# Optimization experiments

Measured on AMD Instinct MI355X. Metric: run time of the kernel, lower is better.

The kernel has to match this reference:

```python
import jax, jax.numpy as jnp
import numpy as np

N = 200000
M = 100000
K = 27
C = 128
NEG_SLOPE = 0.2


def setup_inputs() -> dict:
    key = jax.random.key(0)
    ks = jax.random.split(key, 7)
    feats = jax.random.normal(ks[0], (N, C), dtype=jnp.float32)
    # small init scale (mirrors xavier * 0.1) to keep activations stable through 27-tap convs
    W1 = jax.random.normal(ks[1], (K, C, C), dtype=jnp.float32) * 0.02
    W2 = jax.random.normal(ks[2], (C, C), dtype=jnp.float32) * 0.05
    W3 = jax.random.normal(ks[3], (K, C, C), dtype=jnp.float32) * 0.02
    in_map = jax.random.randint(ks[4], (K, M), 0, N, dtype=jnp.int32)
    out_map = jax.random.randint(ks[5], (K, M), 0, N, dtype=jnp.int32)
    mask = jax.random.uniform(ks[6], (N, 1), dtype=jnp.float32)
    return {"feats": feats, "W1": W1, "W2": W2, "W3": W3,
            "in_map": in_map, "out_map": out_map, "mask": mask}


def _lrelu(x):
    return jnp.where(x >= 0, x, NEG_SLOPE * x)


def _sparse_conv(feats, W, in_map, out_map, n_out):
    """Gather-GEMM-scatter sparse conv: scan over K kernel offsets.

    feats: [N, Cin]; W: [K, Cin, Cout]; in_map/out_map: [K, M].
    """
    def body(acc, xs):
        im, om, w = xs
        y = feats[im] @ w                    # [M, Cin] @ [Cin, Cout]
        return acc.at[om].add(y), None
    out0 = jnp.zeros((n_out, W.shape[-1]), feats.dtype)
    out, _ = jax.lax.scan(body, out0, (in_map, out_map, W))
    return out


def reference(feats, W1, W2, W3, in_map, out_map, mask):
    n = feats.shape[0]
    c1 = _lrelu(_sparse_conv(feats, W1, in_map, out_map, n))   # conv1 (k=3) + LeakyReLU
    c2 = _lrelu(c1 @ W2)                                       # conv2 (k=1) + LeakyReLU
    c3 = _sparse_conv(c2, W3, in_map, out_map, n)              # conv3 (k=3)
    return c3 * mask
```

## Files before the change

### kernel.cpp

```cpp
#include <hip/hip_runtime.h>
#include <hip/hip_bf16.h>


typedef __attribute__((ext_vector_type(8))) short short8;
typedef __attribute__((ext_vector_type(4))) float f32x4;

#define CDIM 128
#define BM   128
#define NEG_SLOPE 0.2f

__device__ __forceinline__ unsigned short f2bf(float x) {
    union { float f; unsigned u; } un; un.f = x;
    unsigned r = un.u + 0x7fffu + ((un.u >> 16) & 1u);
    return (unsigned short)(r >> 16);
}

__device__ __forceinline__ float lrelu(float x) {
    return x >= 0.f ? x : NEG_SLOPE * x;
}

__device__ __forceinline__ int swz(int r, int c) {
    return (r << 7) + ((((c >> 3) ^ (r & 15)) << 3));
}

__global__ void cvt_feats_kernel(const float* __restrict__ in,
                                 unsigned short* __restrict__ out, int n4) {
    int i = blockIdx.x * blockDim.x + threadIdx.x;
    if (i >= n4) return;
    float4 v = reinterpret_cast<const float4*>(in)[i];
    ushort4 o;
    o.x = f2bf(v.x); o.y = f2bf(v.y); o.z = f2bf(v.z); o.w = f2bf(v.w);
    reinterpret_cast<ushort4*>(out)[i] = o;
}

__global__ void cvt_weights_kernel(const float* __restrict__ W1,
                                   const float* __restrict__ W2,
                                   const float* __restrict__ W3,
                                   unsigned short* __restrict__ W1t,
                                   unsigned short* __restrict__ W2t,
                                   unsigned short* __restrict__ W3t) {
    const int KW = 27 * 128 * 128;
    int t = blockIdx.x * blockDim.x + threadIdx.x;
    if (t < KW) {
        int k = t >> 14, r = t & 16383, n = r >> 7, kk = r & 127;
        W1t[t] = f2bf(W1[(k << 14) + (kk << 7) + n]);
    } else if (t < 2 * KW) {
        int t2 = t - KW;
        int k = t2 >> 14, r = t2 & 16383, n = r >> 7, kk = r & 127;
        W3t[t2] = f2bf(W3[(k << 14) + (kk << 7) + n]);
    } else if (t < 2 * KW + 16384) {
        int t2 = t - 2 * KW;
        int n = t2 >> 7, kk = t2 & 127;
        W2t[t2] = f2bf(W2[(kk << 7) + n]);
    }
}

__global__ __launch_bounds__(256, 2)
void sconv_kernel(const unsigned short* __restrict__ A,
                  const unsigned short* __restrict__ Wt,
                  const int* __restrict__ in_map,
                  const int* __restrict__ out_map,
                  float* __restrict__ out,
                  int M) {
    const int k     = blockIdx.y;
    const int mbase = blockIdx.x * BM;
    const int tid   = threadIdx.x;

    __shared__ unsigned short lA[BM * CDIM];
    __shared__ unsigned short lW[CDIM * CDIM];

    const unsigned short* wk = Wt + (size_t)k * 16384;
    #pragma unroll
    for (int i = 0; i < 8; ++i) {
        int flat = (i * 256 + tid) * 8;
        int row = flat >> 7, col = flat & 127;
        short8 v = *reinterpret_cast<const short8*>(wk + flat);
        *reinterpret_cast<short8*>(&lW[swz(row, col)]) = v;
    }

    const int* imk = in_map + (size_t)k * M;
    #pragma unroll
    for (int p = 0; p < 8; ++p) {
        int r = p * 16 + (tid >> 4);
        int c = (tid & 15) * 8;
        int m = mbase + r;
        short8 v = {0, 0, 0, 0, 0, 0, 0, 0};
        if (m < M) {
            int arow = __ldg(imk + m);
            v = *reinterpret_cast<const short8*>(A + (size_t)arow * CDIM + c);
        }
        *reinterpret_cast<short8*>(&lA[swz(r, c)]) = v;
    }
    __syncthreads();

    const int wid  = tid >> 6, lane = tid & 63;
    const int wr   = (wid >> 1) * 64, wc = (wid & 1) * 64;
    const int lrow = lane & 15, quad = lane >> 4;

    f32x4 acc[4][4];
    #pragma unroll
    for (int i = 0; i < 4; ++i)
        #pragma unroll
        for (int j = 0; j < 4; ++j)
            acc[i][j] = {0.f, 0.f, 0.f, 0.f};

    #pragma unroll
    for (int s = 0; s < 4; ++s) {
        const int kf = s * 32 + quad * 8;
        short8 a[4], b[4];
        #pragma unroll
        for (int i = 0; i < 4; ++i)
            a[i] = *reinterpret_cast<const short8*>(&lA[swz(wr + i * 16 + lrow, kf)]);
        #pragma unroll
        for (int j = 0; j < 4; ++j)
            b[j] = *reinterpret_cast<const short8*>(&lW[swz(wc + j * 16 + lrow, kf)]);
        #pragma unroll
        for (int i = 0; i < 4; ++i)
            #pragma unroll
            for (int j = 0; j < 4; ++j)
                acc[i][j] = __builtin_amdgcn_mfma_f32_16x16x32_bf16(a[i], b[j], acc[i][j], 0, 0, 0);
    }

    const int* omk = out_map + (size_t)k * M;
    #pragma unroll
    for (int i = 0; i < 4; ++i) {
        #pragma unroll
        for (int reg = 0; reg < 4; ++reg) {
            int m = mbase + wr + i * 16 + quad * 4 + reg;
            if (m < M) {
                int orow = __ldg(omk + m);
                float* dst = out + (size_t)orow * CDIM + wc + lrow;
                #pragma unroll
                for (int j = 0; j < 4; ++j)
                    unsafeAtomicAdd(dst + j * 16, acc[i][j][reg]);
            }
        }
    }
}

__global__ __launch_bounds__(256, 2)
void conv2_kernel(const float* __restrict__ c1,
                  const unsigned short* __restrict__ W2t,
                  unsigned short* __restrict__ c2,
                  int M) {
    const int mbase = blockIdx.x * BM;
    const int tid   = threadIdx.x;

    __shared__ unsigned short lA[BM * CDIM];
    __shared__ unsigned short lW[CDIM * CDIM];

    #pragma unroll
    for (int i = 0; i < 8; ++i) {
        int flat = (i * 256 + tid) * 8;
        int row = flat >> 7, col = flat & 127;
        short8 v = *reinterpret_cast<const short8*>(W2t + flat);
        *reinterpret_cast<short8*>(&lW[swz(row, col)]) = v;
    }

    #pragma unroll
    for (int p = 0; p < 8; ++p) {
        int r = p * 16 + (tid >> 4);
        int c = (tid & 15) * 8;
        int m = mbase + r;
        unsigned short vv[8];
        if (m < M) {
            const float4* src = reinterpret_cast<const float4*>(c1 + (size_t)m * CDIM + c);
            float4 x0 = src[0], x1 = src[1];
            vv[0] = f2bf(lrelu(x0.x)); vv[1] = f2bf(lrelu(x0.y));
            vv[2] = f2bf(lrelu(x0.z)); vv[3] = f2bf(lrelu(x0.w));
            vv[4] = f2bf(lrelu(x1.x)); vv[5] = f2bf(lrelu(x1.y));
            vv[6] = f2bf(lrelu(x1.z)); vv[7] = f2bf(lrelu(x1.w));
        } else {
            #pragma unroll
            for (int q = 0; q < 8; ++q) vv[q] = 0;
        }
        short8 v;
        #pragma unroll
        for (int q = 0; q < 8; ++q) v[q] = (short)vv[q];
        *reinterpret_cast<short8*>(&lA[swz(r, c)]) = v;
    }
    __syncthreads();

    const int wid  = tid >> 6, lane = tid & 63;
    const int wr   = (wid >> 1) * 64, wc = (wid & 1) * 64;
    const int lrow = lane & 15, quad = lane >> 4;

    f32x4 acc[4][4];
    #pragma unroll
    for (int i = 0; i < 4; ++i)
        #pragma unroll
        for (int j = 0; j < 4; ++j)
            acc[i][j] = {0.f, 0.f, 0.f, 0.f};

    #pragma unroll
    for (int s = 0; s < 4; ++s) {
        const int kf = s * 32 + quad * 8;
        short8 a[4], b[4];
        #pragma unroll
        for (int i = 0; i < 4; ++i)
            a[i] = *reinterpret_cast<const short8*>(&lA[swz(wr + i * 16 + lrow, kf)]);
        #pragma unroll
        for (int j = 0; j < 4; ++j)
            b[j] = *reinterpret_cast<const short8*>(&lW[swz(wc + j * 16 + lrow, kf)]);
        #pragma unroll
        for (int i = 0; i < 4; ++i)
            #pragma unroll
            for (int j = 0; j < 4; ++j)
                acc[i][j] = __builtin_amdgcn_mfma_f32_16x16x32_bf16(a[i], b[j], acc[i][j], 0, 0, 0);
    }

    #pragma unroll
    for (int i = 0; i < 4; ++i) {
        #pragma unroll
        for (int reg = 0; reg < 4; ++reg) {
            int m = mbase + wr + i * 16 + quad * 4 + reg;
            if (m < M) {
                unsigned short* dst = c2 + (size_t)m * CDIM + wc + lrow;
                #pragma unroll
                for (int j = 0; j < 4; ++j)
                    dst[j * 16] = f2bf(lrelu(acc[i][j][reg]));
            }
        }
    }
}

__global__ void mask_mul_kernel(float* __restrict__ out,
                                const float* __restrict__ mask, int n4) {
    int i = blockIdx.x * blockDim.x + threadIdx.x;
    if (i >= n4) return;
    int row = i >> 5;
    float m = mask[row];
    float4 v = reinterpret_cast<float4*>(out)[i];
    v.x *= m; v.y *= m; v.z *= m; v.w *= m;
    reinterpret_cast<float4*>(out)[i] = v;
}

extern "C" void kernel_launch(void* const* d_in, const int* in_sizes, int n_in,
                              void* d_out, int out_size, void* d_ws, size_t ws_size,
                              hipStream_t stream) {
    const float* feats   = (const float*)d_in[0];
    const float* W1      = (const float*)d_in[1];
    const float* W2      = (const float*)d_in[2];
    const float* W3      = (const float*)d_in[3];
    const int*   in_map  = (const int*)d_in[4];
    const int*   out_map = (const int*)d_in[5];
    const float* mask    = (const float*)d_in[6];
    float*       out     = (float*)d_out;

    const int K = 27;
    const int N = in_sizes[0] / CDIM;
    const int M = in_sizes[4] / K;

    unsigned short* feats_bf = (unsigned short*)d_ws;
    unsigned short* c2_bf    = feats_bf + (size_t)N * CDIM;
    unsigned short* W1t      = c2_bf + (size_t)N * CDIM;
    unsigned short* W3t      = W1t + (size_t)K * CDIM * CDIM;
    unsigned short* W2t      = W3t + (size_t)K * CDIM * CDIM;
    size_t need = ((size_t)2 * N * CDIM + (size_t)2 * K * CDIM * CDIM + CDIM * CDIM) * 2;
    if (ws_size < need) return;

    const int n4 = N * CDIM / 4;
    cvt_feats_kernel<<<(n4 + 255) / 256, 256, 0, stream>>>(feats, feats_bf, n4);
    const int wtot = 2 * K * CDIM * CDIM + CDIM * CDIM;
    cvt_weights_kernel<<<(wtot + 255) / 256, 256, 0, stream>>>(W1, W2, W3, W1t, W2t, W3t);

    hipMemsetAsync(d_out, 0, (size_t)N * CDIM * sizeof(float), stream);

    dim3 gs((M + BM - 1) / BM, K);
    sconv_kernel<<<gs, 256, 0, stream>>>(feats_bf, W1t, in_map, out_map, out, M);

    conv2_kernel<<<(N + BM - 1) / BM, 256, 0, stream>>>(out, W2t, c2_bf, N);

    hipMemsetAsync(d_out, 0, (size_t)N * CDIM * sizeof(float), stream);
    sconv_kernel<<<gs, 256, 0, stream>>>(c2_bf, W3t, in_map, out_map, out, M);

    mask_mul_kernel<<<(n4 + 255) / 256, 256, 0, stream>>>(out, mask, n4);
}
```

Baseline: 2.534 ms.

## Bin gather records by output tile and accumulate sparse conv in LDS

Adds histogram, scan and scatter passes that bucket every (in, out) pair by 64-row output tile and kernel tap. A new output-stationary kernel then gathers inputs, runs the MFMA GEMM per tap and accumulates into a shared-memory tile with LDS atomics, instead of issuing float atomics to global memory. conv2 with its LeakyReLU, and the final mask multiply, are fused into the tile epilogue, which removes the output memsets and separate passes. The cost is re-staging the weights per tap for every tile, small uneven GEMMs per bin, extra preprocessing kernels, and heavy LDS use that limits occupancy.

```diff
diff --git a/kernel.cpp b/kernel.cpp
--- a/kernel.cpp
+++ b/kernel.cpp
@@ -6,7 +6,8 @@
 typedef __attribute__((ext_vector_type(4))) float f32x4;
 
 #define CDIM 128
-#define BM   128
+#define TROWS 64
+#define KTAPS 27
 #define NEG_SLOPE 0.2f
 
 __device__ __forceinline__ unsigned short f2bf(float x) {
@@ -39,7 +40,7 @@
                                    unsigned short* __restrict__ W1t,
                                    unsigned short* __restrict__ W2t,
                                    unsigned short* __restrict__ W3t) {
-    const int KW = 27 * 128 * 128;
+    const int KW = KTAPS * CDIM * CDIM;
     int t = blockIdx.x * blockDim.x + threadIdx.x;
     if (t < KW) {
         int k = t >> 14, r = t & 16383, n = r >> 7, kk = r & 127;
@@ -48,191 +49,201 @@
         int t2 = t - KW;
         int k = t2 >> 14, r = t2 & 16383, n = r >> 7, kk = r & 127;
         W3t[t2] = f2bf(W3[(k << 14) + (kk << 7) + n]);
-    } else if (t < 2 * KW + 16384) {
+    } else if (t < 2 * KW + CDIM * CDIM) {
         int t2 = t - 2 * KW;
         int n = t2 >> 7, kk = t2 & 127;
         W2t[t2] = f2bf(W2[(kk << 7) + n]);
     }
 }
 
+__global__ void hist_kernel(const int* __restrict__ om, int* __restrict__ bins, int M) {
+    int m = blockIdx.x * 256 + threadIdx.x;
+    int k = blockIdx.y;
+    if (m >= M) return;
+    int o = om[(size_t)k * M + m];
+    atomicAdd(&bins[(o >> 6) * KTAPS + k], 1);
+}
+
+__global__ void scan_kernel(const int* __restrict__ bins, int* __restrict__ starts, int B) {
+    __shared__ int lds[1024];
+    int t = threadIdx.x;
+    int seg = (B + 1023) >> 10;
+    int base = t * seg;
+    int s = 0;
+    for (int i = 0; i < seg; ++i) { int idx = base + i; if (idx < B) s += bins[idx]; }
+    lds[t] = s;
+    __syncthreads();
+    for (int off = 1; off < 1024; off <<= 1) {
+        int v = lds[t];
+        int add = (t >= off) ? lds[t - off] : 0;
+        __syncthreads();
+        lds[t] = v + add;
+        __syncthreads();
+    }
+    int run = (t == 0) ? 0 : lds[t - 1];
+    for (int i = 0; i < seg; ++i) {
+        int idx = base + i;
+        if (idx < B) { starts[idx] = run; run += bins[idx]; }
+    }
+    if (t == 1023) starts[B] = lds[1023];
+}
+
+__global__ void scatter_kernel(const int* __restrict__ im, const int* __restrict__ om,
+                               const int* __restrict__ starts, int* __restrict__ cursor,
+                               unsigned* __restrict__ rec, int M) {
+    int m = blockIdx.x * 256 + threadIdx.x;
+    int k = blockIdx.y;
+    if (m >= M) return;
+    size_t e = (size_t)k * M + m;
+    int o = om[e];
+    int bin = (o >> 6) * KTAPS + k;
+    int pos = starts[bin] + atomicAdd(&cursor[bin], 1);
+    rec[pos] = ((unsigned)im[e] << 6) | (unsigned)(o & 63);
+}
+
 __global__ __launch_bounds__(256, 2)
-void sconv_kernel(const unsigned short* __restrict__ A,
-                  const unsigned short* __restrict__ Wt,
-                  const int* __restrict__ in_map,
-                  const int* __restrict__ out_map,
-                  float* __restrict__ out,
-                  int M) {
-    const int k     = blockIdx.y;
-    const int mbase = blockIdx.x * BM;
-    const int tid   = threadIdx.x;
-
-    __shared__ unsigned short lA[BM * CDIM];
+void sconv_inv_kernel(const unsigned short* __restrict__ A,
+                      const unsigned short* __restrict__ Wt,
+                      const unsigned* __restrict__ rec,
+                      const int* __restrict__ starts,
+                      const unsigned short* __restrict__ W2t,
+                      unsigned short* __restrict__ c2,
+                      const float* __restrict__ mask,
+                      float* __restrict__ outp,
+                      int mode) {
+    __shared__ float          accW[TROWS * CDIM];
+    __shared__ unsigned short lA[TROWS * CDIM];
     __shared__ unsigned short lW[CDIM * CDIM];
 
-    const unsigned short* wk = Wt + (size_t)k * 16384;
+    const int t    = blockIdx.x;
+    const int tid  = threadIdx.x;
+    const int w    = tid >> 6;
+    const int lane = tid & 63;
+    const int lrow = lane & 15;
+    const int quad = lane >> 4;
+
     #pragma unroll
-    for (int i = 0; i < 8; ++i) {
-        int flat = (i * 256 + tid) * 8;
-        int row = flat >> 7, col = flat & 127;
-        short8 v = *reinterpret_cast<const short8*>(wk + flat);
-        *reinterpret_cast<short8*>(&lW[swz(row, col)]) = v;
-    }
-
-    const int* imk = in_map + (size_t)k * M;
-    #pragma unroll
-    for (int p = 0; p < 8; ++p) {
-        int r = p * 16 + (tid >> 4);
-        int c = (tid & 15) * 8;
-        int m = mbase + r;
-        short8 v = {0, 0, 0, 0, 0, 0, 0, 0};
-        if (m < M) {
-            int arow = __ldg(imk + m);
-            v = *reinterpret_cast<const short8*>(A + (size_t)arow * CDIM + c);
-        }
-        *reinterpret_cast<short8*>(&lA[swz(r, c)]) = v;
+    for (int i = 0; i < 8; ++i)
+        reinterpret_cast<float4*>(accW)[i * 256 + tid] = make_float4(0.f, 0.f, 0.f, 0.f);
+
+    for (int k = 0; k < KTAPS; ++k) {
+        __syncthreads();
+        const unsigned short* wk = Wt + (size_t)k * (CDIM * CDIM);
+        #pragma unroll
+        for (int i = 0; i < 8; ++i) {
+            int flat = (i * 256 + tid) * 8;
+            int row = flat >> 7, col = flat & 127;
+            *reinterpret_cast<short8*>(&lW[swz(row, col)]) =
+                *reinterpret_cast<const short8*>(wk + flat);
+        }
+        const int bin = t * KTAPS + k;
+        const int s0  = starts[bin];
+        const int cnt = starts[bin + 1] - s0;
+
+        for (int base = 0; base < cnt; base += TROWS) {
+            int c = cnt - base; if (c > TROWS) c = TROWS;
+            if (base > 0) __syncthreads();
+            #pragma unroll
+            for (int p = 0; p < 4; ++p) {
+                int r = p * 16 + (tid >> 4);
+                if (r < c) {
+                    unsigned rv = rec[s0 + base + r];
+                    int src = (int)(rv >> 6);
+                    *reinterpret_cast<short8*>(&lA[swz(r, (tid & 15) * 8)]) =
+                        *reinterpret_cast<const short8*>(A + (size_t)src * CDIM + (tid & 15) * 8);
+                }
+            }
+            __syncthreads();
+            int r16 = (c + 15) >> 4;
+            short8 b0[4], b1[4];
+            #pragma unroll
+            for (int kf = 0; kf < 4; ++kf) {
+                b0[kf] = *reinterpret_cast<const short8*>(&lW[swz(w * 32 + lrow,      kf * 32 + quad * 8)]);
+                b1[kf] = *reinterpret_cast<const short8*>(&lW[swz(w * 32 + 16 + lrow, kf * 32 + quad * 8)]);
+            }
+            for (int rt = 0; rt < r16; ++rt) {
+                f32x4 acc0 = {0.f, 0.f, 0.f, 0.f}, acc1 = {0.f, 0.f, 0.f, 0.f};
+                #pragma unroll
+                for (int kf = 0; kf < 4; ++kf) {
+                    short8 av = *reinterpret_cast<const short8*>(&lA[swz(rt * 16 + lrow, kf * 32 + quad * 8)]);
+                    acc0 = __builtin_amdgcn_mfma_f32_16x16x32_bf16(av, b0[kf], acc0, 0, 0, 0);
+                    acc1 = __builtin_amdgcn_mfma_f32_16x16x32_bf16(av, b1[kf], acc1, 0, 0, 0);
+                }
+                #pragma unroll
+                for (int reg = 0; reg < 4; ++reg) {
+                    int rr = rt * 16 + quad * 4 + reg;
+                    if (rr < c) {
+                        int slot = (int)(rec[s0 + base + rr] & 63u);
+                        atomicAdd(&accW[slot * CDIM + w * 32 + lrow],      acc0[reg]);
+                        atomicAdd(&accW[slot * CDIM + w * 32 + 16 + lrow], acc1[reg]);
+                    }
+                }
+            }
+        }
     }
     __syncthreads();
 
-    const int wid  = tid >> 6, lane = tid & 63;
-    const int wr   = (wid >> 1) * 64, wc = (wid & 1) * 64;
-    const int lrow = lane & 15, quad = lane >> 4;
-
-    f32x4 acc[4][4];
-    #pragma unroll
-    for (int i = 0; i < 4; ++i)
-        #pragma unroll
-        for (int j = 0; j < 4; ++j)
-            acc[i][j] = {0.f, 0.f, 0.f, 0.f};
-
-    #pragma unroll
-    for (int s = 0; s < 4; ++s) {
-        const int kf = s * 32 + quad * 8;
-        short8 a[4], b[4];
-        #pragma unroll
-        for (int i = 0; i < 4; ++i)
-            a[i] = *reinterpret_cast<const short8*>(&lA[swz(wr + i * 16 + lrow, kf)]);
-        #pragma unroll
-        for (int j = 0; j < 4; ++j)
-            b[j] = *reinterpret_cast<const short8*>(&lW[swz(wc + j * 16 + lrow, kf)]);
-        #pragma unroll
-        for (int i = 0; i < 4; ++i)
-            #pragma unroll
-            for (int j = 0; j < 4; ++j)
-                acc[i][j] = __builtin_amdgcn_mfma_f32_16x16x32_bf16(a[i], b[j], acc[i][j], 0, 0, 0);
-    }
-
-    const int* omk = out_map + (size_t)k * M;
-    #pragma unroll
-    for (int i = 0; i < 4; ++i) {
-        #pragma unroll
-        for (int reg = 0; reg < 4; ++reg) {
-            int m = mbase + wr + i * 16 + quad * 4 + reg;
-            if (m < M) {
-                int orow = __ldg(omk + m);
-                float* dst = out + (size_t)orow * CDIM + wc + lrow;
-                #pragma unroll
-                for (int j = 0; j < 4; ++j)
-                    unsafeAtomicAdd(dst + j * 16, acc[i][j][reg]);
-            }
-        }
-    }
-}
-
-__global__ __launch_bounds__(256, 2)
-void conv2_kernel(const float* __restrict__ c1,
-                  const unsigned short* __restrict__ W2t,
-                  unsigned short* __restrict__ c2,
-                  int M) {
-    const int mbase = blockIdx.x * BM;
-    const int tid   = threadIdx.x;
-
-    __shared__ unsigned short lA[BM * CDIM];
-    __shared__ unsigned short lW[CDIM * CDIM];
-
-    #pragma unroll
-    for (int i = 0; i < 8; ++i) {
-        int flat = (i * 256 + tid) * 8;
-        int row = flat >> 7, col = flat & 127;
-        short8 v = *reinterpret_cast<const short8*>(W2t + flat);
-        *reinterpret_cast<short8*>(&lW[swz(row, col)]) = v;
-    }
-
-    #pragma unroll
-    for (int p = 0; p < 8; ++p) {
-        int r = p * 16 + (tid >> 4);
-        int c = (tid & 15) * 8;
-        int m = mbase + r;
-        unsigned short vv[8];
-        if (m < M) {
-            const float4* src = reinterpret_cast<const float4*>(c1 + (size_t)m * CDIM + c);
-            float4 x0 = src[0], x1 = src[1];
-            vv[0] = f2bf(lrelu(x0.x)); vv[1] = f2bf(lrelu(x0.y));
-            vv[2] = f2bf(lrelu(x0.z)); vv[3] = f2bf(lrelu(x0.w));
-            vv[4] = f2bf(lrelu(x1.x)); vv[5] = f2bf(lrelu(x1.y));
-            vv[6] = f2bf(lrelu(x1.z)); vv[7] = f2bf(lrelu(x1.w));
-        } else {
-            #pragma unroll
-            for (int q = 0; q < 8; ++q) vv[q] = 0;
-        }
-        short8 v;
-        #pragma unroll
-        for (int q = 0; q < 8; ++q) v[q] = (short)vv[q];
-        *reinterpret_cast<short8*>(&lA[swz(r, c)]) = v;
-    }
-    __syncthreads();
-
-    const int wid  = tid >> 6, lane = tid & 63;
-    const int wr   = (wid >> 1) * 64, wc = (wid & 1) * 64;
-    const int lrow = lane & 15, quad = lane >> 4;
-
-    f32x4 acc[4][4];
-    #pragma unroll
-    for (int i = 0; i < 4; ++i)
-        #pragma unroll
-        for (int j = 0; j < 4; ++j)
-            acc[i][j] = {0.f, 0.f, 0.f, 0.f};
-
-    #pragma unroll
-    for (int s = 0; s < 4; ++s) {
-        const int kf = s * 32 + quad * 8;
-        short8 a[4], b[4];
-        #pragma unroll
-        for (int i = 0; i < 4; ++i)
-            a[i] = *reinterpret_cast<const short8*>(&lA[swz(wr + i * 16 + lrow, kf)]);
-        #pragma unroll
-        for (int j = 0; j < 4; ++j)
-            b[j] = *reinterpret_cast<const short8*>(&lW[swz(wc + j * 16 + lrow, kf)]);
-        #pragma unroll
-        for (int i = 0; i < 4; ++i)
-            #pragma unroll
-            for (int j = 0; j < 4; ++j)
-                acc[i][j] = __builtin_amdgcn_mfma_f32_16x16x32_bf16(a[i], b[j], acc[i][j], 0, 0, 0);
-    }
-
-    #pragma unroll
-    for (int i = 0; i < 4; ++i) {
-        #pragma unroll
-        for (int reg = 0; reg < 4; ++reg) {
-            int m = mbase + wr + i * 16 + quad * 4 + reg;
-            if (m < M) {
-                unsigned short* dst = c2 + (size_t)m * CDIM + wc + lrow;
-                #pragma unroll
-                for (int j = 0; j < 4; ++j)
-                    dst[j * 16] = f2bf(lrelu(acc[i][j][reg]));
-            }
-        }
-    }
-}
-
-__global__ void mask_mul_kernel(float* __restrict__ out,
-                                const float* __restrict__ mask, int n4) {
-    int i = blockIdx.x * blockDim.x + threadIdx.x;
-    if (i >= n4) return;
-    int row = i >> 5;
-    float m = mask[row];
-    float4 v = reinterpret_cast<float4*>(out)[i];
-    v.x *= m; v.y *= m; v.z *= m; v.w *= m;
-    reinterpret_cast<float4*>(out)[i] = v;
+    if (mode == 1) {
+        #pragma unroll
+        for (int i = 0; i < 8; ++i) {
+            int flat = (i * 256 + tid) * 8;
+            int row = flat >> 7, col = flat & 127;
+            *reinterpret_cast<short8*>(&lW[swz(row, col)]) =
+                *reinterpret_cast<const short8*>(W2t + flat);
+        }
+        {
+            int row = tid >> 2, c0 = (tid & 3) * 32;
+            #pragma unroll
+            for (int j = 0; j < 4; ++j) {
+                const float4* sp = reinterpret_cast<const float4*>(accW + row * CDIM + c0 + j * 8);
+                float4 x0 = sp[0], x1 = sp[1];
+                short8 v;
+                v[0] = (short)f2bf(lrelu(x0.x)); v[1] = (short)f2bf(lrelu(x0.y));
+                v[2] = (short)f2bf(lrelu(x0.z)); v[3] = (short)f2bf(lrelu(x0.w));
+                v[4] = (short)f2bf(lrelu(x1.x)); v[5] = (short)f2bf(lrelu(x1.y));
+                v[6] = (short)f2bf(lrelu(x1.z)); v[7] = (short)f2bf(lrelu(x1.w));
+                *reinterpret_cast<short8*>(&lA[swz(row, c0 + j * 8)]) = v;
+            }
+        }
+        __syncthreads();
+        unsigned short* cacc = reinterpret_cast<unsigned short*>(accW);
+        #pragma unroll
+        for (int rt = 0; rt < 4; ++rt) {
+            f32x4 acc0 = {0.f, 0.f, 0.f, 0.f}, acc1 = {0.f, 0.f, 0.f, 0.f};
+            #pragma unroll
+            for (int kf = 0; kf < 4; ++kf) {
+                short8 av = *reinterpret_cast<const short8*>(&lA[swz(rt * 16 + lrow, kf * 32 + quad * 8)]);
+                short8 b0 = *reinterpret_cast<const short8*>(&lW[swz(w * 32 + lrow,      kf * 32 + quad * 8)]);
+                short8 b1 = *reinterpret_cast<const short8*>(&lW[swz(w * 32 + 16 + lrow, kf * 32 + quad * 8)]);
+                acc0 = __builtin_amdgcn_mfma_f32_16x16x32_bf16(av, b0, acc0, 0, 0, 0);
+                acc1 = __builtin_amdgcn_mfma_f32_16x16x32_bf16(av, b1, acc1, 0, 0, 0);
+            }
+            #pragma unroll
+            for (int reg = 0; reg < 4; ++reg) {
+                int rr = rt * 16 + quad * 4 + reg;
+                cacc[rr * CDIM + w * 32 + lrow]      = f2bf(lrelu(acc0[reg]));
+                cacc[rr * CDIM + w * 32 + 16 + lrow] = f2bf(lrelu(acc1[reg]));
+            }
+        }
+        __syncthreads();
+        #pragma unroll
+        for (int i = 0; i < 4; ++i) {
+            int flat = (i * 256 + tid) * 8;
+            *reinterpret_cast<short8*>(c2 + (size_t)t * TROWS * CDIM + flat) =
+                *reinterpret_cast<const short8*>(cacc + flat);
+        }
+    } else {
+        int row = tid >> 2, c0 = (tid & 3) * 32;
+        float mval = mask[t * TROWS + row];
+        const float4* sp = reinterpret_cast<const float4*>(accW + row * CDIM + c0);
+        float4* dp = reinterpret_cast<float4*>(outp + (size_t)t * TROWS * CDIM + row * CDIM + c0);
+        #pragma unroll
+        for (int j = 0; j < 8; ++j) {
+            float4 v = sp[j];
+            v.x *= mval; v.y *= mval; v.z *= mval; v.w *= mval;
+            dp[j] = v;
+        }
+    }
 }
 
 extern "C" void kernel_launch(void* const* d_in, const int* in_sizes, int n_in,
@@ -247,32 +258,38 @@
     const float* mask    = (const float*)d_in[6];
     float*       out     = (float*)d_out;
 
-    const int K = 27;
-    const int N = in_sizes[0] / CDIM;
-    const int M = in_sizes[4] / K;
-
-    unsigned short* feats_bf = (unsigned short*)d_ws;
-    unsigned short* c2_bf    = feats_bf + (size_t)N * CDIM;
-    unsigned short* W1t      = c2_bf + (size_t)N * CDIM;
-    unsigned short* W3t      = W1t + (size_t)K * CDIM * CDIM;
-    unsigned short* W2t      = W3t + (size_t)K * CDIM * CDIM;
-    size_t need = ((size_t)2 * N * CDIM + (size_t)2 * K * CDIM * CDIM + CDIM * CDIM) * 2;
-    if (ws_size < need) return;
+    const int N  = in_sizes[0] / CDIM;
+    const int M  = in_sizes[4] / KTAPS;
+    const int NT = (N + TROWS - 1) / TROWS;
+    const int B  = NT * KTAPS;
+    const size_t E = (size_t)KTAPS * M;
+
+    char* p = (char*)d_ws;
+    auto take = [&](size_t bytes) { char* r = p; p += (bytes + 15) & ~(size_t)15; return r; };
+    unsigned short* feats_bf = (unsigned short*)take((size_t)N * CDIM * 2);
+    unsigned short* c2_bf    = (unsigned short*)take((size_t)N * CDIM * 2);
+    unsigned short* W1t      = (unsigned short*)take((size_t)KTAPS * CDIM * CDIM * 2);
+    unsigned short* W3t      = (unsigned short*)take((size_t)KTAPS * CDIM * CDIM * 2);
+    unsigned short* W2t      = (unsigned short*)take((size_t)CDIM * CDIM * 2);
+    int*            bins     = (int*)take((size_t)(B + 1) * 4);
+    int*            starts   = (int*)take((size_t)(B + 1) * 4);
+    unsigned*       rec      = (unsigned*)take(E * 4);
+    if ((size_t)(p - (char*)d_ws) > ws_size) return;
 
     const int n4 = N * CDIM / 4;
     cvt_feats_kernel<<<(n4 + 255) / 256, 256, 0, stream>>>(feats, feats_bf, n4);
-    const int wtot = 2 * K * CDIM * CDIM + CDIM * CDIM;
+    const int wtot = 2 * KTAPS * CDIM * CDIM + CDIM * CDIM;
     cvt_weights_kernel<<<(wtot + 255) / 256, 256, 0, stream>>>(W1, W2, W3, W1t, W2t, W3t);
 
-    hipMemsetAsync(d_out, 0, (size_t)N * CDIM * sizeof(float), stream);
-
-    dim3 gs((M + BM - 1) / BM, K);
-    sconv_kernel<<<gs, 256, 0, stream>>>(feats_bf, W1t, in_map, out_map, out, M);
-
-    conv2_kernel<<<(N + BM - 1) / BM, 256, 0, stream>>>(out, W2t, c2_bf, N);
-
-    hipMemsetAsync(d_out, 0, (size_t)N * CDIM * sizeof(float), stream);
-    sconv_kernel<<<gs, 256, 0, stream>>>(c2_bf, W3t, in_map, out_map, out, M);
-
-    mask_mul_kernel<<<(n4 + 255) / 256, 256, 0, stream>>>(out, mask, n4);
-}
+    hipMemsetAsync(bins, 0, (size_t)(B + 1) * 4, stream);
+    dim3 gm((M + 255) / 256, KTAPS);
+    hist_kernel<<<gm, 256, 0, stream>>>(out_map, bins, M);
+    scan_kernel<<<1, 1024, 0, stream>>>(bins, starts, B);
+    hipMemsetAsync(bins, 0, (size_t)(B + 1) * 4, stream);
+    scatter_kernel<<<gm, 256, 0, stream>>>(in_map, out_map, starts, bins, rec, M);
+
+    sconv_inv_kernel<<<NT, 256, 0, stream>>>(feats_bf, W1t, rec, starts,
+                                             W2t, c2_bf, nullptr, nullptr, 1);
+    sconv_inv_kernel<<<NT, 256, 0, stream>>>(c2_bf, W3t, rec, starts,
+                                             nullptr, nullptr, mask, out, 2);
+}
```

After: 4.864 ms. 1.92x slower.

## Replace atomic scatter with sorted-record segmented reduction over bf16 per-tap GEMM outputs

Applied to the files above, without the earlier changes.

Replaces the float atomic scatter-add with a deterministic pipeline. A histogram, scan and scatter build a CSR list of contributions per output row, grouped by tap chunks. The per-tap GEMMs write bf16 results to a workspace buffer, and a row-wise reduce kernel sums each output row's contributions, with mask multiply and a channel permutation folded into the final pass. This is meant to remove atomic contention and the extra memset and mask passes. In exchange it adds preprocessing kernels, a large intermediate write/read, and extra bf16 rounding of partial products.

```diff
diff --git a/kernel.cpp b/kernel.cpp
--- a/kernel.cpp
+++ b/kernel.cpp
@@ -6,7 +6,7 @@
 typedef __attribute__((ext_vector_type(4))) float f32x4;
 
 #define CDIM 128
-#define BM   128
+#define KTAPS 27
 #define NEG_SLOPE 0.2f
 
 __device__ __forceinline__ unsigned short f2bf(float x) {
@@ -14,14 +14,11 @@
     unsigned r = un.u + 0x7fffu + ((un.u >> 16) & 1u);
     return (unsigned short)(r >> 16);
 }
-
-__device__ __forceinline__ float lrelu(float x) {
-    return x >= 0.f ? x : NEG_SLOPE * x;
-}
-
-__device__ __forceinline__ int swz(int r, int c) {
-    return (r << 7) + ((((c >> 3) ^ (r & 15)) << 3));
-}
+__device__ __forceinline__ float bflo(unsigned v) { union { unsigned u; float f; } un; un.u = v << 16; return un.f; }
+__device__ __forceinline__ float bfhi(unsigned v) { union { unsigned u; float f; } un; un.u = v & 0xffff0000u; return un.f; }
+__device__ __forceinline__ float lrelu(float x) { return x >= 0.f ? x : NEG_SLOPE * x; }
+__device__ __forceinline__ int swz(int r, int c) { return (r << 7) + ((((c >> 3) ^ (r & 15)) << 3)); }
+__device__ __forceinline__ int pcol(int q) { return (q & 64) | ((q & 3) << 4) | ((q >> 2) & 15); }
 
 __global__ void cvt_feats_kernel(const float* __restrict__ in,
                                  unsigned short* __restrict__ out, int n4) {
@@ -38,35 +35,81 @@
                                    const float* __restrict__ W3,
                                    unsigned short* __restrict__ W1t,
                                    unsigned short* __restrict__ W2t,
-                                   unsigned short* __restrict__ W3t) {
-    const int KW = 27 * 128 * 128;
+                                   unsigned short* __restrict__ W3t, int perm) {
+    const int KW = KTAPS * CDIM * CDIM;
     int t = blockIdx.x * blockDim.x + threadIdx.x;
     if (t < KW) {
         int k = t >> 14, r = t & 16383, n = r >> 7, kk = r & 127;
         W1t[t] = f2bf(W1[(k << 14) + (kk << 7) + n]);
     } else if (t < 2 * KW) {
         int t2 = t - KW;
-        int k = t2 >> 14, r = t2 & 16383, n = r >> 7, kk = r & 127;
+        int k = t2 >> 14, r = t2 & 16383, n = r >> 7, q = r & 127;
+        int kk = perm ? pcol(q) : q;
         W3t[t2] = f2bf(W3[(k << 14) + (kk << 7) + n]);
-    } else if (t < 2 * KW + 16384) {
+    } else if (t < 2 * KW + CDIM * CDIM) {
         int t2 = t - 2 * KW;
-        int n = t2 >> 7, kk = t2 & 127;
+        int n = t2 >> 7, q = t2 & 127;
+        int kk = perm ? pcol(q) : q;
         W2t[t2] = f2bf(W2[(kk << 7) + n]);
     }
 }
 
+__global__ void hist_kernel(const int* __restrict__ om, int* __restrict__ bins,
+                            int M, int ng, int g) {
+    int m = blockIdx.x * 256 + threadIdx.x;
+    int k = blockIdx.y;
+    if (m >= M) return;
+    int o = om[(size_t)k * M + m];
+    atomicAdd(&bins[o * ng + k / g], 1);
+}
+
+__global__ void scan_kernel(const int* __restrict__ bins, int* __restrict__ starts, int B) {
+    __shared__ int lds[1024];
+    int t = threadIdx.x;
+    int seg = (B + 1023) >> 10;
+    int base = t * seg;
+    int s = 0;
+    for (int i = 0; i < seg; ++i) { int idx = base + i; if (idx < B) s += bins[idx]; }
+    lds[t] = s;
+    __syncthreads();
+    for (int off = 1; off < 1024; off <<= 1) {
+        int v = lds[t];
+        int add = (t >= off) ? lds[t - off] : 0;
+        __syncthreads();
+        lds[t] = v + add;
+        __syncthreads();
+    }
+    int run = (t == 0) ? 0 : lds[t - 1];
+    for (int i = 0; i < seg; ++i) {
+        int idx = base + i;
+        if (idx < B) { starts[idx] = run; run += bins[idx]; }
+    }
+    if (t == 1023) starts[B] = lds[1023];
+}
+
+__global__ void scatter_kernel(const int* __restrict__ om,
+                               const int* __restrict__ starts, int* __restrict__ cursor,
+                               unsigned* __restrict__ rec, int M, int ng, int g) {
+    int m = blockIdx.x * 256 + threadIdx.x;
+    int k = blockIdx.y;
+    if (m >= M) return;
+    int o = om[(size_t)k * M + m];
+    int bin = o * ng + k / g;
+    int pos = starts[bin] + atomicAdd(&cursor[bin], 1);
+    rec[pos] = (unsigned)(k * M + m);
+}
+
 __global__ __launch_bounds__(256, 2)
-void sconv_kernel(const unsigned short* __restrict__ A,
-                  const unsigned short* __restrict__ Wt,
-                  const int* __restrict__ in_map,
-                  const int* __restrict__ out_map,
-                  float* __restrict__ out,
-                  int M) {
-    const int k     = blockIdx.y;
-    const int mbase = blockIdx.x * BM;
+void gemm_gather_kernel(const unsigned short* __restrict__ A,
+                        const unsigned short* __restrict__ Wt,
+                        const int* __restrict__ in_map,
+                        unsigned short* __restrict__ Y,
+                        int M, int klo) {
+    const int k     = klo + blockIdx.y;
+    const int mbase = blockIdx.x * 128;
     const int tid   = threadIdx.x;
 
-    __shared__ unsigned short lA[BM * CDIM];
+    __shared__ unsigned short lA[128 * CDIM];
     __shared__ unsigned short lW[CDIM * CDIM];
 
     const unsigned short* wk = Wt + (size_t)k * 16384;
@@ -74,10 +117,9 @@
     for (int i = 0; i < 8; ++i) {
         int flat = (i * 256 + tid) * 8;
         int row = flat >> 7, col = flat & 127;
-        short8 v = *reinterpret_cast<const short8*>(wk + flat);
-        *reinterpret_cast<short8*>(&lW[swz(row, col)]) = v;
-    }
-
+        *reinterpret_cast<short8*>(&lW[swz(row, col)]) =
+            *reinterpret_cast<const short8*>(wk + flat);
+    }
     const int* imk = in_map + (size_t)k * M;
     #pragma unroll
     for (int p = 0; p < 8; ++p) {
@@ -93,8 +135,214 @@
     }
     __syncthreads();
 
-    const int wid  = tid >> 6, lane = tid & 63;
-    const int wr   = (wid >> 1) * 64, wc = (wid & 1) * 64;
+    const int wid = tid >> 6, lane = tid & 63;
+    const int wr = (wid >> 1) * 64, wc = (wid & 1) * 64;
+    const int lrow = lane & 15, quad = lane >> 4;
+
+    f32x4 acc[4][4];
+    #pragma unroll
+    for (int i = 0; i < 4; ++i)
+        #pragma unroll
+        for (int j = 0; j < 4; ++j)
+            acc[i][j] = {0.f, 0.f, 0.f, 0.f};
+
+    #pragma unroll
+    for (int s = 0; s < 4; ++s) {
+        const int kf = s * 32 + quad * 8;
+        short8 a[4], b[4];
+        #pragma unroll
+        for (int i = 0; i < 4; ++i)
+            a[i] = *reinterpret_cast<const short8*>(&lA[swz(wr + i * 16 + lrow, kf)]);
+        #pragma unroll
+        for (int j = 0; j < 4; ++j)
+            b[j] = *reinterpret_cast<const short8*>(&lW[swz(wc + j * 16 + lrow, kf)]);
+        #pragma unroll
+        for (int i = 0; i < 4; ++i)
+            #pragma unroll
+            for (int j = 0; j < 4; ++j)
+                acc[i][j] = __builtin_amdgcn_mfma_f32_16x16x32_bf16(a[i], b[j], acc[i][j], 0, 0, 0);
+    }
+
+    const size_t ybase = (size_t)(k - klo) * M;
+    #pragma unroll
+    for (int i = 0; i < 4; ++i) {
+        #pragma unroll
+        for (int reg = 0; reg < 4; ++reg) {
+            int m = mbase + wr + i * 16 + quad * 4 + reg;
+            if (m < M) {
+                ushort4 pk;
+                pk.x = f2bf(acc[i][0][reg]);
+                pk.y = f2bf(acc[i][1][reg]);
+                pk.z = f2bf(acc[i][2][reg]);
+                pk.w = f2bf(acc[i][3][reg]);
+                *reinterpret_cast<ushort4*>(Y + (ybase + m) * CDIM + wc + lrow * 4) = pk;
+            }
+        }
+    }
+}
+
+__global__ void reduce_kernel(const unsigned short* __restrict__ Y,
+                              const unsigned* __restrict__ rec,
+                              const int* __restrict__ starts,
+                              float* __restrict__ acc,
+                              const float* __restrict__ mask,
+                              int N, int ng, int grp, unsigned eoff,
+                              int first, int final_mask) {
+    int row = blockIdx.x * 4 + (threadIdx.x >> 6);
+    if (row >= N) return;
+    int lane = threadIdx.x & 63;
+    int bin = row * ng + grp;
+    int s0 = starts[bin], cnt = starts[bin + 1] - s0;
+    float a0 = 0.f, a1 = 0.f;
+    if (!first) {
+        float2 p = *reinterpret_cast<const float2*>(acc + (size_t)row * CDIM + 2 * lane);
+        a0 = p.x; a1 = p.y;
+    }
+    const unsigned* rp = rec + s0;
+    int c = 0;
+    for (; c + 4 <= cnt; c += 4) {
+        unsigned e0 = rp[c] - eoff, e1 = rp[c + 1] - eoff;
+        unsigned e2 = rp[c + 2] - eoff, e3 = rp[c + 3] - eoff;
+        unsigned v0 = *reinterpret_cast<const unsigned*>(Y + (size_t)e0 * CDIM + 2 * lane);
+        unsigned v1 = *reinterpret_cast<const unsigned*>(Y + (size_t)e1 * CDIM + 2 * lane);
+        unsigned v2 = *reinterpret_cast<const unsigned*>(Y + (size_t)e2 * CDIM + 2 * lane);
+        unsigned v3 = *reinterpret_cast<const unsigned*>(Y + (size_t)e3 * CDIM + 2 * lane);
+        a0 += (bflo(v0) + bflo(v1)) + (bflo(v2) + bflo(v3));
+        a1 += (bfhi(v0) + bfhi(v1)) + (bfhi(v2) + bfhi(v3));
+    }
+    for (; c < cnt; ++c) {
+        unsigned e = rp[c] - eoff;
+        unsigned v = *reinterpret_cast<const unsigned*>(Y + (size_t)e * CDIM + 2 * lane);
+        a0 += bflo(v); a1 += bfhi(v);
+    }
+    if (!final_mask) {
+        *reinterpret_cast<float2*>(acc + (size_t)row * CDIM + 2 * lane) = make_float2(a0, a1);
+    } else {
+        float mv = mask[row];
+        acc[(size_t)row * CDIM + pcol(2 * lane)]     = a0 * mv;
+        acc[(size_t)row * CDIM + pcol(2 * lane + 1)] = a1 * mv;
+    }
+}
+
+__global__ __launch_bounds__(256, 2)
+void conv2_perm_kernel(const float* __restrict__ c1,
+                       const unsigned short* __restrict__ W2t,
+                       unsigned short* __restrict__ c2,
+                       int N) {
+    const int mbase = blockIdx.x * 128;
+    const int tid   = threadIdx.x;
+
+    __shared__ unsigned short lA[128 * CDIM];
+    __shared__ unsigned short lW[CDIM * CDIM];
+
+    #pragma unroll
+    for (int i = 0; i < 8; ++i) {
+        int flat = (i * 256 + tid) * 8;
+        int row = flat >> 7, col = flat & 127;
+        *reinterpret_cast<short8*>(&lW[swz(row, col)]) =
+            *reinterpret_cast<const short8*>(W2t + flat);
+    }
+    #pragma unroll
+    for (int p = 0; p < 8; ++p) {
+        int r = p * 16 + (tid >> 4);
+        int c = (tid & 15) * 8;
+        int m = mbase + r;
+        short8 v = {0, 0, 0, 0, 0, 0, 0, 0};
+        if (m < N) {
+            const float4* src = reinterpret_cast<const float4*>(c1 + (size_t)m * CDIM + c);
+            float4 x0 = src[0], x1 = src[1];
+            v[0] = (short)f2bf(lrelu(x0.x)); v[1] = (short)f2bf(lrelu(x0.y));
+            v[2] = (short)f2bf(lrelu(x0.z)); v[3] = (short)f2bf(lrelu(x0.w));
+            v[4] = (short)f2bf(lrelu(x1.x)); v[5] = (short)f2bf(lrelu(x1.y));
+            v[6] = (short)f2bf(lrelu(x1.z)); v[7] = (short)f2bf(lrelu(x1.w));
+        }
+        *reinterpret_cast<short8*>(&lA[swz(r, c)]) = v;
+    }
+    __syncthreads();
+
+    const int wid = tid >> 6, lane = tid & 63;
+    const int wr = (wid >> 1) * 64, wc = (wid & 1) * 64;
+    const int lrow = lane & 15, quad = lane >> 4;
+
+    f32x4 acc[4][4];
+    #pragma unroll
+    for (int i = 0; i < 4; ++i)
+        #pragma unroll
+        for (int j = 0; j < 4; ++j)
+            acc[i][j] = {0.f, 0.f, 0.f, 0.f};
+
+    #pragma unroll
+    for (int s = 0; s < 4; ++s) {
+        const int kf = s * 32 + quad * 8;
+        short8 a[4], b[4];
+        #pragma unroll
+        for (int i = 0; i < 4; ++i)
+            a[i] = *reinterpret_cast<const short8*>(&lA[swz(wr + i * 16 + lrow, kf)]);
+        #pragma unroll
+        for (int j = 0; j < 4; ++j)
+            b[j] = *reinterpret_cast<const short8*>(&lW[swz(wc + j * 16 + lrow, kf)]);
+        #pragma unroll
+        for (int i = 0; i < 4; ++i)
+            #pragma unroll
+            for (int j = 0; j < 4; ++j)
+                acc[i][j] = __builtin_amdgcn_mfma_f32_16x16x32_bf16(a[i], b[j], acc[i][j], 0, 0, 0);
+    }
+
+    #pragma unroll
+    for (int i = 0; i < 4; ++i) {
+        #pragma unroll
+        for (int reg = 0; reg < 4; ++reg) {
+            int m = mbase + wr + i * 16 + quad * 4 + reg;
+            if (m < N) {
+                ushort4 pk;
+                pk.x = f2bf(lrelu(acc[i][0][reg]));
+                pk.y = f2bf(lrelu(acc[i][1][reg]));
+                pk.z = f2bf(lrelu(acc[i][2][reg]));
+                pk.w = f2bf(lrelu(acc[i][3][reg]));
+                *reinterpret_cast<ushort4*>(c2 + (size_t)m * CDIM + wc + lrow * 4) = pk;
+            }
+        }
+    }
+}
+
+__global__ __launch_bounds__(256, 2)
+void sconv_atomic_kernel(const unsigned short* __restrict__ A,
+                         const unsigned short* __restrict__ Wt,
+                         const int* __restrict__ in_map,
+                         const int* __restrict__ out_map,
+                         float* __restrict__ out, int M) {
+    const int k     = blockIdx.y;
+    const int mbase = blockIdx.x * 128;
+    const int tid   = threadIdx.x;
+
+    __shared__ unsigned short lA[128 * CDIM];
+    __shared__ unsigned short lW[CDIM * CDIM];
+
+    const unsigned short* wk = Wt + (size_t)k * 16384;
+    #pragma unroll
+    for (int i = 0; i < 8; ++i) {
+        int flat = (i * 256 + tid) * 8;
+        int row = flat >> 7, col = flat & 127;
+        *reinterpret_cast<short8*>(&lW[swz(row, col)]) =
+            *reinterpret_cast<const short8*>(wk + flat);
+    }
+    const int* imk = in_map + (size_t)k * M;
+    #pragma unroll
+    for (int p = 0; p < 8; ++p) {
+        int r = p * 16 + (tid >> 4);
+        int c = (tid & 15) * 8;
+        int m = mbase + r;
+        short8 v = {0, 0, 0, 0, 0, 0, 0, 0};
+        if (m < M) {
+            int arow = __ldg(imk + m);
+            v = *reinterpret_cast<const short8*>(A + (size_t)arow * CDIM + c);
+        }
+        *reinterpret_cast<short8*>(&lA[swz(r, c)]) = v;
+    }
+    __syncthreads();
+
+    const int wid = tid >> 6, lane = tid & 63;
+    const int wr = (wid >> 1) * 64, wc = (wid & 1) * 64;
     const int lrow = lane & 15, quad = lane >> 4;
 
     f32x4 acc[4][4];
@@ -139,50 +387,42 @@
 }
 
 __global__ __launch_bounds__(256, 2)
-void conv2_kernel(const float* __restrict__ c1,
-                  const unsigned short* __restrict__ W2t,
-                  unsigned short* __restrict__ c2,
-                  int M) {
-    const int mbase = blockIdx.x * BM;
+void conv2_true_kernel(const float* __restrict__ c1,
+                       const unsigned short* __restrict__ W2t,
+                       unsigned short* __restrict__ c2, int N) {
+    const int mbase = blockIdx.x * 128;
     const int tid   = threadIdx.x;
 
-    __shared__ unsigned short lA[BM * CDIM];
+    __shared__ unsigned short lA[128 * CDIM];
     __shared__ unsigned short lW[CDIM * CDIM];
 
     #pragma unroll
     for (int i = 0; i < 8; ++i) {
         int flat = (i * 256 + tid) * 8;
         int row = flat >> 7, col = flat & 127;
-        short8 v = *reinterpret_cast<const short8*>(W2t + flat);
-        *reinterpret_cast<short8*>(&lW[swz(row, col)]) = v;
-    }
-
+        *reinterpret_cast<short8*>(&lW[swz(row, col)]) =
+            *reinterpret_cast<const short8*>(W2t + flat);
+    }
     #pragma unroll
     for (int p = 0; p < 8; ++p) {
         int r = p * 16 + (tid >> 4);
         int c = (tid & 15) * 8;
         int m = mbase + r;
-        unsigned short vv[8];
-        if (m < M) {
+        short8 v = {0, 0, 0, 0, 0, 0, 0, 0};
+        if (m < N) {
             const float4* src = reinterpret_cast<const float4*>(c1 + (size_t)m * CDIM + c);
             float4 x0 = src[0], x1 = src[1];
-            vv[0] = f2bf(lrelu(x0.x)); vv[1] = f2bf(lrelu(x0.y));
-            vv[2] = f2bf(lrelu(x0.z)); vv[3] = f2bf(lrelu(x0.w));
-            vv[4] = f2bf(lrelu(x1.x)); vv[5] = f2bf(lrelu(x1.y));
-            vv[6] = f2bf(lrelu(x1.z)); vv[7] = f2bf(lrelu(x1.w));
-        } else {
-            #pragma unroll
-            for (int q = 0; q < 8; ++q) vv[q] = 0;
-        }
-        short8 v;
-        #pragma unroll
-        for (int q = 0; q < 8; ++q) v[q] = (short)vv[q];
+            v[0] = (short)f2bf(lrelu(x0.x)); v[1] = (short)f2bf(lrelu(x0.y));
+            v[2] = (short)f2bf(lrelu(x0.z)); v[3] = (short)f2bf(lrelu(x0.w));
+            v[4] = (short)f2bf(lrelu(x1.x)); v[5] = (short)f2bf(lrelu(x1.y));
+            v[6] = (short)f2bf(lrelu(x1.z)); v[7] = (short)f2bf(lrelu(x1.w));
+        }
         *reinterpret_cast<short8*>(&lA[swz(r, c)]) = v;
     }
     __syncthreads();
 
-    const int wid  = tid >> 6, lane = tid & 63;
-    const int wr   = (wid >> 1) * 64, wc = (wid & 1) * 64;
+    const int wid = tid >> 6, lane = tid & 63;
+    const int wr = (wid >> 1) * 64, wc = (wid & 1) * 64;
     const int lrow = lane & 15, quad = lane >> 4;
 
     f32x4 acc[4][4];
@@ -214,7 +454,7 @@
         #pragma unroll
         for (int reg = 0; reg < 4; ++reg) {
             int m = mbase + wr + i * 16 + quad * 4 + reg;
-            if (m < M) {
+            if (m < N) {
                 unsigned short* dst = c2 + (size_t)m * CDIM + wc + lrow;
                 #pragma unroll
                 for (int j = 0; j < 4; ++j)
@@ -247,32 +487,77 @@
     const float* mask    = (const float*)d_in[6];
     float*       out     = (float*)d_out;
 
-    const int K = 27;
     const int N = in_sizes[0] / CDIM;
-    const int M = in_sizes[4] / K;
-
-    unsigned short* feats_bf = (unsigned short*)d_ws;
-    unsigned short* c2_bf    = feats_bf + (size_t)N * CDIM;
-    unsigned short* W1t      = c2_bf + (size_t)N * CDIM;
-    unsigned short* W3t      = W1t + (size_t)K * CDIM * CDIM;
-    unsigned short* W2t      = W3t + (size_t)K * CDIM * CDIM;
-    size_t need = ((size_t)2 * N * CDIM + (size_t)2 * K * CDIM * CDIM + CDIM * CDIM) * 2;
-    if (ws_size < need) return;
+    const int M = in_sizes[4] / KTAPS;
+    const size_t E = (size_t)KTAPS * M;
+
+    auto al = [](size_t b) { return (b + 255) & ~(size_t)255; };
+    size_t featsB = al((size_t)N * CDIM * 2);
+    size_t c2B    = al((size_t)N * CDIM * 2);
+    size_t w1B    = al((size_t)KTAPS * CDIM * CDIM * 2);
+    size_t w2B    = al((size_t)CDIM * CDIM * 2);
+    size_t recB   = al(E * 4);
+    size_t base   = featsB + c2B + 2 * w1B + w2B + recB;
+
+    int g = 0, ng = 0;
+    for (int gg = KTAPS; gg >= 1; --gg) {
+        int n_g = (KTAPS + gg - 1) / gg;
+        size_t need = base + 2 * al(((size_t)N * n_g + 1) * 4) + al((size_t)gg * M * CDIM * 2);
+        if (need <= ws_size) { g = gg; ng = n_g; break; }
+    }
+
+    char* p = (char*)d_ws;
+    auto take = [&](size_t b) { char* r = p; p += al(b); return r; };
+    unsigned short* feats_bf = (unsigned short*)take((size_t)N * CDIM * 2);
+    unsigned short* c2_bf    = (unsigned short*)take((size_t)N * CDIM * 2);
+    unsigned short* W1t      = (unsigned short*)take((size_t)KTAPS * CDIM * CDIM * 2);
+    unsigned short* W3t      = (unsigned short*)take((size_t)KTAPS * CDIM * CDIM * 2);
+    unsigned short* W2t      = (unsigned short*)take((size_t)CDIM * CDIM * 2);
+    unsigned*       rec      = (unsigned*)take(E * 4);
 
     const int n4 = N * CDIM / 4;
     cvt_feats_kernel<<<(n4 + 255) / 256, 256, 0, stream>>>(feats, feats_bf, n4);
-    const int wtot = 2 * K * CDIM * CDIM + CDIM * CDIM;
-    cvt_weights_kernel<<<(wtot + 255) / 256, 256, 0, stream>>>(W1, W2, W3, W1t, W2t, W3t);
-
-    hipMemsetAsync(d_out, 0, (size_t)N * CDIM * sizeof(float), stream);
-
-    dim3 gs((M + BM - 1) / BM, K);
-    sconv_kernel<<<gs, 256, 0, stream>>>(feats_bf, W1t, in_map, out_map, out, M);
-
-    conv2_kernel<<<(N + BM - 1) / BM, 256, 0, stream>>>(out, W2t, c2_bf, N);
-
-    hipMemsetAsync(d_out, 0, (size_t)N * CDIM * sizeof(float), stream);
-    sconv_kernel<<<gs, 256, 0, stream>>>(c2_bf, W3t, in_map, out_map, out, M);
-
-    mask_mul_kernel<<<(n4 + 255) / 256, 256, 0, stream>>>(out, mask, n4);
-}
+    const int wtot = 2 * KTAPS * CDIM * CDIM + CDIM * CDIM;
+    cvt_weights_kernel<<<(wtot + 255) / 256, 256, 0, stream>>>(W1, W2, W3, W1t, W2t, W3t, g ? 1 : 0);
+
+    const int MT = (M + 127) / 128;
+    dim3 gm((M + 255) / 256, KTAPS);
+
+    if (g) {
+        int B = N * ng;
+        int* bins   = (int*)take(((size_t)B + 1) * 4);
+        int* starts = (int*)take(((size_t)B + 1) * 4);
+        unsigned short* Ybuf = (unsigned short*)take((size_t)g * M * CDIM * 2);
+
+        hipMemsetAsync(bins, 0, ((size_t)B + 1) * 4, stream);
+        hist_kernel<<<gm, 256, 0, stream>>>(out_map, bins, M, ng, g);
+        scan_kernel<<<1, 1024, 0, stream>>>(bins, starts, B);
+        hipMemsetAsync(bins, 0, ((size_t)B + 1) * 4, stream);
+        scatter_kernel<<<gm, 256, 0, stream>>>(out_map, starts, bins, rec, M, ng, g);
+
+        const int rgrid = (N + 3) / 4;
+        for (int grp = 0; grp < ng; ++grp) {
+            int klo = grp * g;
+            int kh  = klo + g; if (kh > KTAPS) kh = KTAPS;
+            gemm_gather_kernel<<<dim3(MT, kh - klo), 256, 0, stream>>>(feats_bf, W1t, in_map, Ybuf, M, klo);
+            reduce_kernel<<<rgrid, 256, 0, stream>>>(Ybuf, rec, starts, out, nullptr,
+                                                     N, ng, grp, (unsigned)(klo * M), grp == 0, 0);
+        }
+        conv2_perm_kernel<<<(N + 127) / 128, 256, 0, stream>>>(out, W2t, c2_bf, N);
+        for (int grp = 0; grp < ng; ++grp) {
+            int klo = grp * g;
+            int kh  = klo + g; if (kh > KTAPS) kh = KTAPS;
+            gemm_gather_kernel<<<dim3(MT, kh - klo), 256, 0, stream>>>(c2_bf, W3t, in_map, Ybuf, M, klo);
+            reduce_kernel<<<rgrid, 256, 0, stream>>>(Ybuf, rec, starts, out, mask,
+                                                     N, ng, grp, (unsigned)(klo * M), grp == 0, grp == ng - 1);
+        }
+    } else {
+        hipMemsetAsync(out, 0, (size_t)N * CDIM * 4, stream);
+        dim3 gs(MT, KTAPS);
+        sconv_atomic_kernel<<<gs, 256, 0, stream>>>(feats_bf, W1t, in_map, out_map, out, M);
+        conv2_true_kernel<<<(N + 127) / 128, 256, 0, stream>>>(out, W2t, c2_bf, N);
+        hipMemsetAsync(out, 0, (size_t)N * CDIM * 4, stream);
+        sconv_atomic_kernel<<<gs, 256, 0, stream>>>(c2_bf, W3t, in_map, out_map, out, M);
+        mask_mul_kernel<<<(n4 + 255) / 256, 256, 0, stream>>>(out, mask, n4);
+    }
+}
```

Measured after the change: 3.269 ms. 29.0% more time.
